# Kernel optimization log

Hardware: AMD Instinct MI355X
Metric: run time of the kernel (lower is better)

The kernel has to match this reference:

```python
import jax, jax.numpy as jnp
import numpy as np

STRIDES = [8, 16, 32, 64, 128]
FEAT_SIZES = [(100, 100), (50, 50), (25, 25), (13, 13), (7, 7)]
IMG_H, IMG_W = 800, 800
NUM_CLASSES = 8  # required by the repeat(8) in _loss_single_scale
BATCH, NUM_GT = 8, 50


def _make_anchor_levels():
    """RetinaNet anchors: octave_base_scale=4, scales_per_octave=3, ratios [0.5,1,2]."""
    ratios = np.array([0.5, 1.0, 2.0], dtype=np.float64)
    scales = 4.0 * 2.0 ** (np.arange(3) / 3.0)
    levels = []
    for stride, (fh, fw) in zip(STRIDES, FEAT_SIZES):
        h_r = np.sqrt(ratios)
        w_r = 1.0 / h_r
        ws = (w_r[:, None] * scales[None, :]).reshape(-1) * stride  # [9]
        hs = (h_r[:, None] * scales[None, :]).reshape(-1) * stride
        base = np.stack([-ws / 2, -hs / 2, ws / 2, hs / 2], axis=1)  # [9,4]
        xs = np.arange(fw) * stride
        ys = np.arange(fh) * stride
        xx, yy = np.meshgrid(xs, ys)  # [fh,fw]
        shifts = np.stack([xx, yy, xx, yy], axis=-1).reshape(-1, 4)  # [fh*fw,4]
        anchors = (shifts[:, None, :] + base[None, :, :]).reshape(-1, 4)  # loc-major, A inner
        levels.append(anchors.astype(np.float32))
    return levels


def _pairwise_iou(a, b):
    # a: [K,4], b: [G,4] -> [K,G]
    area_a = (a[:, 2] - a[:, 0]) * (a[:, 3] - a[:, 1])
    area_b = (b[:, 2] - b[:, 0]) * (b[:, 3] - b[:, 1])
    lt = jnp.maximum(a[:, None, :2], b[None, :, :2])
    rb = jnp.minimum(a[:, None, 2:], b[None, :, 2:])
    wh = jnp.clip(rb - lt, 0.0)
    inter = wh[..., 0] * wh[..., 1]
    return inter / (area_a[:, None] + area_b[None, :] - inter)


def _encode(anchors, gts):
    # DeltaXYWH encode, means=0, stds=1
    aw = anchors[:, 2] - anchors[:, 0]
    ah = anchors[:, 3] - anchors[:, 1]
    ax = anchors[:, 0] + 0.5 * aw
    ay = anchors[:, 1] + 0.5 * ah
    gw = gts[:, 2] - gts[:, 0]
    gh = gts[:, 3] - gts[:, 1]
    gx = gts[:, 0] + 0.5 * gw
    gy = gts[:, 1] + 0.5 * gh
    return jnp.stack([(gx - ax) / aw, (gy - ay) / ah,
                      jnp.log(gw / aw), jnp.log(gh / ah)], axis=1)


def _targets_per_image(anchors, tgt_boxes, tgt_cls):
    # MaxIoUMatcher(thresholds=[0.4,0.5], labels=[0,-1,1], low_quality=True)
    inside = ((anchors[:, 0] >= 0) & (anchors[:, 1] >= 0)
              & (anchors[:, 2] <= IMG_W) & (anchors[:, 3] <= IMG_H))
    iou = _pairwise_iou(anchors, tgt_boxes)             # [K,G]
    iou = jnp.where(inside[:, None], iou, -1.0)          # exclude outside anchors
    max_iou = iou.max(axis=1)
    argmax_gt = iou.argmax(axis=1)
    label = jnp.where(max_iou >= 0.5, 1, jnp.where(max_iou >= 0.4, -1, 0))
    gt_max = iou.max(axis=0)                             # [G]
    is_lq = (iou == gt_max[None, :]) & (gt_max[None, :] > 0)
    any_lq = is_lq.any(axis=1)
    G = tgt_boxes.shape[0]
    lq_gt = jnp.where(is_lq, jnp.arange(G)[None, :], -1).max(axis=1)
    matched_gt = jnp.where(any_lq, lq_gt, argmax_gt)
    label = jnp.where(any_lq, 1, label)
    pos = (label == 1) & inside
    neg = (label == 0) & inside
    deltas = _encode(anchors, tgt_boxes[matched_gt])     # [K,4]
    bbox_targets = jnp.where(pos[:, None], deltas, 0.0)
    bbox_weights = jnp.where(pos[:, None], 1.0, 0.0) * jnp.ones((1, 4), jnp.float32)
    labels_out = jnp.where(pos, tgt_cls[matched_gt].astype(jnp.float32), 0.0)
    label_weights = (pos | neg).astype(jnp.float32)
    return labels_out, label_weights, bbox_targets, bbox_weights, pos.sum(), neg.sum()


def _bce_logits(x, t):
    return jnp.maximum(x, 0.0) - x * t + jnp.log1p(jnp.exp(-jnp.abs(x)))


def _loss_level(cls_out, reg_out, labels, lw, bt, bw, num_samples):
    labels = labels.reshape(-1)
    lw = lw.reshape(-1)
    C = NUM_CLASSES
    cls_score = cls_out.transpose(0, 2, 3, 1).reshape(labels.shape[0], C)  # [N*H*W*A, C]
    tgt = jax.nn.one_hot(labels.astype(jnp.int32), C + 1, dtype=jnp.float32)[:, :C]
    lw2 = jnp.tile(lw, 8).reshape(-1, C)  # faithful to label_weights.repeat(8).reshape(-1, C)
    loss_cls = (_bce_logits(cls_score, tgt) * lw2).sum() / num_samples
    bt = bt.reshape(-1, 4)
    bw = bw.reshape(-1, 4)
    pred = reg_out.transpose(0, 2, 3, 1).reshape(-1, 4)
    loss_bbox = (jnp.abs(pred - bt) * bw).sum() / num_samples
    return loss_cls, loss_bbox


def setup_inputs() -> dict:
    key = jax.random.key(0)
    ks = jax.random.split(key, 16)
    inp = {}
    for i, (fh, fw) in enumerate(FEAT_SIZES):
        inp[f"cls{i}"] = jax.random.normal(ks[i], (BATCH, 9 * NUM_CLASSES, fh, fw), jnp.float32)
        inp[f"reg{i}"] = jax.random.normal(ks[5 + i], (BATCH, 9 * 4, fh, fw), jnp.float32)
    xy = jax.random.uniform(ks[10], (BATCH, NUM_GT, 2), minval=0.0, maxval=600.0)
    wh = jax.random.uniform(ks[11], (BATCH, NUM_GT, 2), minval=20.0, maxval=180.0)
    inp["target_boxes"] = jnp.concatenate([xy, xy + wh], axis=-1).astype(jnp.float32)
    inp["target_class_ids"] = jax.random.randint(ks[12], (BATCH, NUM_GT), 0, NUM_CLASSES, jnp.int64 if jax.config.jax_enable_x64 else jnp.int32)
    return inp


def reference(cls0, cls1, cls2, cls3, cls4, reg0, reg1, reg2, reg3, reg4,
              target_boxes, target_class_ids):
    anchor_levels = _make_anchor_levels()
    anchors = jnp.asarray(np.concatenate(anchor_levels, axis=0))  # [K,4]
    num_lvl = [a.shape[0] for a in anchor_levels]
    labels, lw, bt, bw, npos, nneg = jax.vmap(
        lambda b, c: _targets_per_image(anchors, b, c))(target_boxes, target_class_ids)
    num_samples = (npos.sum() + nneg.sum()).astype(jnp.float32)
    offs = np.cumsum([0] + num_lvl)
    cls_outs = [cls0, cls1, cls2, cls3, cls4]
    reg_outs = [reg0, reg1, reg2, reg3, reg4]
    loss_cls_all = jnp.float32(0.0)
    loss_bbox_all = jnp.float32(0.0)
    for i in range(len(num_lvl)):
        s, e = int(offs[i]), int(offs[i + 1])
        lc, lb = _loss_level(cls_outs[i], reg_outs[i], labels[:, s:e], lw[:, s:e],
                             bt[:, s:e], bw[:, s:e], num_samples)
        loss_cls_all = loss_cls_all + lc
        loss_bbox_all = loss_bbox_all + lb
    return loss_cls_all, loss_bbox_all
```

## Files before the change

kernel.cpp:

```cpp
#include <hip/hip_runtime.h>
#include <cstdint>

#define DEVINL __device__ __forceinline__

constexpr int NB = 8;
constexpr int NG = 50;
constexpr int KTOT = 120087;
constexpr int BK = NB * KTOT;

constexpr int L_W[5]   = {100, 50, 25, 13, 7};
constexpr int L_K[5]   = {90000, 22500, 5625, 1521, 441};
constexpr int L_OFF[5] = {0, 90000, 112500, 118125, 119646};
constexpr int L_WSB[5] = {0, 720000, 900000, 945000, 957168};

constexpr double HR_T[3] = {0.7071067811865476, 1.0, 1.4142135623730951};
constexpr double WR_T[3] = {1.0 / HR_T[0], 1.0, 1.0 / HR_T[2]};
constexpr double SC_T[3] = {4.0, 5.039684199579493, 6.3496042078727974};

__device__ float4 g_anc[KTOT];
__device__ double g_accs[256][2];
__device__ unsigned g_ns;
__device__ unsigned g_done;
__device__ unsigned g_gtmax[NB * NG];
__device__ int8_t g_lab[BK];
__device__ __align__(8) int8_t g_lw[BK];
__device__ int8_t g_pos[BK];
__device__ int8_t g_mg[BK];

DEVINL unsigned encf(float f) {
  unsigned u = __float_as_uint(f);
  return (u & 0x80000000u) ? ~u : (u | 0x80000000u);
}
DEVINL int lvl_of(int k) {
  return (k < 90000) ? 0 : (k < 112500) ? 1 : (k < 118125) ? 2 : (k < 119646) ? 3 : 4;
}
DEVINL float iou_one(float ax0, float ay0, float ax1, float ay1, float areaA,
                     float bx0, float by0, float bx1, float by1, float areaB) {
  float ltx = fmaxf(ax0, bx0);
  float lty = fmaxf(ay0, by0);
  float rbx = fminf(ax1, bx1);
  float rby = fminf(ay1, by1);
  float wx = fmaxf(rbx - ltx, 0.0f);
  float wy = fmaxf(rby - lty, 0.0f);
  float inter = wx * wy;
  return __fdividef(inter, areaA + areaB - inter);
}

DEVINL void wh_f64(int l, int a, double& wsz, double& hsz) {
  int st = 8 << l;
  int ridx = a / 3, sidx = a - ridx * 3;
  double sc = (sidx == 0) ? SC_T[0] : (sidx == 1) ? SC_T[1] : SC_T[2];
  double wr = (ridx == 0) ? WR_T[0] : (ridx == 1) ? WR_T[1] : WR_T[2];
  double hr = (ridx == 0) ? HR_T[0] : (ridx == 1) ? HR_T[1] : HR_T[2];
  wsz = wr * sc * (double)st;
  hsz = hr * sc * (double)st;
}
DEVINL void anchor_from_wh(int l, int xi, int yi, double wsz, double hsz,
                           float& x0, float& y0, float& x1, float& y1) {
  int st = 8 << l;
  double cx = (double)(xi * st), cy = (double)(yi * st);
  x0 = (float)(cx - wsz * 0.5);
  y0 = (float)(cy - hsz * 0.5);
  x1 = (float)(cx + wsz * 0.5);
  y1 = (float)(cy + hsz * 0.5);
}

constexpr int NBLK_ANC = (KTOT + 255) / 256;

DEVINL int axis_cand(int xi, int i0, int lo, int hi, int Wm1) {
  int c;
  if (xi < 4) c = i0 - 1 + xi;
  else if (xi == 4) c = lo;
  else if (xi == 5) c = lo + 1;
  else if (xi == 6) c = hi - 1;
  else if (xi == 7) c = hi;
  else if (xi == 8) c = 0;
  else c = Wm1;
  return min(max(c, 0), Wm1);
}

__global__ __launch_bounds__(256) void k_setup(const float* __restrict__ tb) {
  if (blockIdx.x < NBLK_ANC) {
    if (blockIdx.x == 0) {
      int t = threadIdx.x;
      g_accs[t][0] = 0.0;
      g_accs[t][1] = 0.0;
      if (t == 0) { g_ns = 0u; g_done = 0u; }
    }
    int k = blockIdx.x * 256 + threadIdx.x;
    if (k >= KTOT) return;
    int l = lvl_of(k);
    int r = k - L_OFF[l];
    int loc = r / 9;
    int a = r - loc * 9;
    int W = L_W[l];
    int y = loc / W;
    int x = loc - y * W;
    double wsz, hsz;
    wh_f64(l, a, wsz, hsz);
    float x0, y0, x1, y1;
    anchor_from_wh(l, x, y, wsz, hsz, x0, y0, x1, y1);
    g_anc[k] = make_float4(x0, y0, x1, y1);
    return;
  }
  const int bg = blockIdx.x - NBLK_ANC;
  float4 v = reinterpret_cast<const float4*>(tb)[bg];
  const float bx0 = v.x, by0 = v.y, bx1 = v.z, by1 = v.w;
  const float areaB = (bx1 - bx0) * (by1 - by0);
  const float bcx = 0.5f * (bx0 + bx1), bcy = 0.5f * (by0 + by1);

  float m = -1.0f;
  for (int t = threadIdx.x; t < 4500; t += 256) {
    int l = t / 900;
    int rem = t - l * 900;
    int a = rem / 100;
    int rem2 = rem - a * 100;
    int xi = rem2 / 10;
    int yi = rem2 - xi * 10;
    int W = (l == 0) ? 100 : (l == 1) ? 50 : (l == 2) ? 25 : (l == 3) ? 13 : 7;
    float stf = (float)(8 << l);
    double wsz, hsz;
    wh_f64(l, a, wsz, hsz);
    float whalf = (float)(wsz * 0.5);
    float hhalf = (float)(hsz * 0.5);
    int i0x = (int)floorf(bcx / stf);
    int lox = (int)ceilf(whalf / stf);
    int hix = (int)floorf((800.0f - whalf) / stf);
    int i0y = (int)floorf(bcy / stf);
    int loy = (int)ceilf(hhalf / stf);
    int hiy = (int)floorf((800.0f - hhalf) / stf);
    int cx = axis_cand(xi, i0x, lox, hix, W - 1);
    int cy = axis_cand(yi, i0y, loy, hiy, W - 1);
    float ax0, ay0, ax1, ay1;
    anchor_from_wh(l, cx, cy, wsz, hsz, ax0, ay0, ax1, ay1);
    bool inside = (ax0 >= 0.0f) & (ay0 >= 0.0f) & (ax1 <= 800.0f) & (ay1 <= 800.0f);
    float areaA = (ax1 - ax0) * (ay1 - ay0);
    float iou = inside ? iou_one(ax0, ay0, ax1, ay1, areaA,
                                 bx0, by0, bx1, by1, areaB)
                       : -1.0f;
    m = fmaxf(m, iou);
  }
#pragma unroll
  for (int off = 32; off; off >>= 1) m = fmaxf(m, __shfl_down(m, off));
  __shared__ float s_m[4];
  int lane = threadIdx.x & 63, wid = threadIdx.x >> 6;
  if (lane == 0) s_m[wid] = m;
  __syncthreads();
  if (threadIdx.x == 0) {
    float r = fmaxf(fmaxf(s_m[0], s_m[1]), fmaxf(s_m[2], s_m[3]));
    g_gtmax[bg] = encf(r);
  }
}

constexpr int APB = 4;
__global__ __launch_bounds__(256) void k_assign(const float* __restrict__ tb,
                                                const int* __restrict__ tcls) {
  const int b = blockIdx.y;
  __shared__ float s_b[NG][8];
  __shared__ int s_cls[NG];
  __shared__ unsigned s_cnt;
  int tid = threadIdx.x;
  if (tid == 0) s_cnt = 0u;
  if (tid < NG) {
    float4 v = reinterpret_cast<const float4*>(tb)[b * NG + tid];
    s_b[tid][0] = v.x; s_b[tid][1] = v.y; s_b[tid][2] = v.z; s_b[tid][3] = v.w;
    s_b[tid][4] = (v.z - v.x) * (v.w - v.y);
    unsigned gm = g_gtmax[b * NG + tid];
    s_b[tid][5] = (gm > 0x80000000u) ? __uint_as_float(gm ^ 0x80000000u)
                                     : __uint_as_float(0x7FC00000u);
    s_cls[tid] = tcls[b * NG + tid];
  }
  __syncthreads();

  const int base = (blockIdx.x * 256 + tid) * APB;
  float Ax0[APB], Ay0[APB], Ax1[APB], Ay1[APB], areaA[APB];
  bool inside[APB];
  float ex0 = __builtin_inff(), ey0 = __builtin_inff();
  float ex1 = -__builtin_inff(), ey1 = -__builtin_inff();
#pragma unroll
  for (int ap = 0; ap < APB; ++ap) {
    int k = base + ap;
    bool valid = k < KTOT;
    float4 A = g_anc[valid ? k : 0];
    bool ins = valid & (A.x >= 0.0f) & (A.y >= 0.0f) & (A.z <= 800.0f) & (A.w <= 800.0f);
    inside[ap] = ins;
    ex0 = fminf(ex0, ins ? A.x : __builtin_inff());
    ey0 = fminf(ey0, ins ? A.y : __builtin_inff());
    ex1 = fmaxf(ex1, ins ? A.z : -__builtin_inff());
    ey1 = fmaxf(ey1, ins ? A.w : -__builtin_inff());
    if (!ins) A = make_float4(-4000.0f, -4000.0f, -3999.0f, -3999.0f);
    Ax0[ap] = A.x; Ay0[ap] = A.y; Ax1[ap] = A.z; Ay1[ap] = A.w;
    areaA[ap] = (A.z - A.x) * (A.w - A.y);
  }
#pragma unroll
  for (int off = 1; off < 64; off <<= 1) {
    ex0 = fminf(ex0, __shfl_xor(ex0, off));
    ey0 = fminf(ey0, __shfl_xor(ey0, off));
    ex1 = fmaxf(ex1, __shfl_xor(ex1, off));
    ey1 = fmaxf(ey1, __shfl_xor(ey1, off));
  }
  unsigned long long amask;
  {
    int g = tid & 63;
    bool act = false;
    if (g < NG) {
      float ox = fminf(ex1, s_b[g][2]) - fmaxf(ex0, s_b[g][0]);
      float oy = fminf(ey1, s_b[g][3]) - fmaxf(ey0, s_b[g][1]);
      act = (ox > 0.0f) && (oy > 0.0f);
    }
    amask = __ballot(act);
  }

  float best[APB];
  int arg[APB], lqg[APB];
#pragma unroll
  for (int ap = 0; ap < APB; ++ap) { best[ap] = -2.0f; arg[ap] = 0; lqg[ap] = -1; }

  while (amask) {
    int g = __builtin_ctzll(amask);
    amask &= amask - 1;
    float gx0 = s_b[g][0], gy0 = s_b[g][1], gx1 = s_b[g][2], gy1 = s_b[g][3];
    float gar = s_b[g][4], qmx = s_b[g][5];
#pragma unroll
    for (int ap = 0; ap < APB; ++ap) {
      float iou = iou_one(Ax0[ap], Ay0[ap], Ax1[ap], Ay1[ap], areaA[ap],
                          gx0, gy0, gx1, gy1, gar);
      if (iou > best[ap]) { best[ap] = iou; arg[ap] = g; }
      if (iou == qmx) lqg[ap] = g;
    }
  }

  int cnt = 0;
#pragma unroll
  for (int ap = 0; ap < APB; ++ap) {
    int k = base + ap;
    if (k < KTOT) {
      int lab = (best[ap] >= 0.5f) ? 1 : ((best[ap] >= 0.4f) ? -1 : 0);
      int mg = arg[ap];
      if (lqg[ap] >= 0) { lab = 1; mg = lqg[ap]; }
      bool pos = (lab == 1) && inside[ap];
      bool neg = (lab == 0) && inside[ap];
      int l = lvl_of(k);
      int r = k - L_OFF[l];
      int widx = L_WSB[l] + b * L_K[l] + r;
      g_lab[widx] = pos ? (int8_t)s_cls[mg] : (int8_t)0;
      g_lw[widx] = (pos || neg) ? 1 : 0;
      g_pos[widx] = pos ? 1 : 0;
      g_mg[widx] = (int8_t)mg;
      cnt += (pos || neg) ? 1 : 0;
    }
  }
#pragma unroll
  for (int off = 32; off; off >>= 1) cnt += __shfl_down(cnt, off);
  if ((tid & 63) == 0 && cnt) atomicAdd(&s_cnt, (unsigned)cnt);
  __syncthreads();
  if (tid == 0 && s_cnt) atomicAdd(&g_ns, s_cnt);
}

constexpr int G_OFF[6] = {0, 180000, 225000, 236304, 239400, 240336};
constexpr int TOTAL_G = 240336;

template <int HW, int GPL, int KL, int WSB, int LOFF>
DEVINL void level_term4(const float* __restrict__ cls, const float* __restrict__ reg,
                        const float4* __restrict__ tb4, int j, float& vc, float& vb) {
  constexpr int NPG = 9 * GPL;
  int b = j / NPG;
  int rem = j - b * NPG;
  int a = rem / GPL;
  int gi = rem - a * GPL;
  int pix0 = gi * 4;
  const float* cb = cls + (b * 72 + a * 8) * HW + pix0;
  const int8_t* lwb = g_lw + WSB + 8 * (9 * pix0 + a);
  int idxb = WSB + b * KL + 9 * pix0 + a;

  if (pix0 + 4 <= HW) {
    float xs[8][4];
#pragma unroll
    for (int c = 0; c < 8; ++c) {
      float4 v4 = *reinterpret_cast<const float4*>(cb + c * HW);
      xs[c][0] = v4.x; xs[c][1] = v4.y; xs[c][2] = v4.z; xs[c][3] = v4.w;
    }
#pragma unroll
    for (int e = 0; e < 4; ++e) {
      unsigned long long lwq =
          *reinterpret_cast<const unsigned long long*>(lwb + 72 * e);
      if (lwq) {
        int lab = g_lab[idxb + 9 * e];
#pragma unroll
        for (int c = 0; c < 8; ++c) {
          float w = (float)((unsigned)(lwq >> (8 * c)) & 0xffu);
          float x = xs[c][e];
          float t = (lab == c) ? 1.0f : 0.0f;
          float ax = fabsf(x);
          float ex = __expf(-ax);
          vc += (fmaxf(x, 0.0f) - x * t + __logf(1.0f + ex)) * w;
        }
      }
      if (g_pos[idxb + 9 * e]) {
        int mg = g_mg[idxb + 9 * e];
        int q = (pix0 + e) * 9 + a;
        float4 A = g_anc[LOFF + q];
        float aw = A.z - A.x, ah = A.w - A.y;
        float acx = A.x + 0.5f * aw, acy = A.y + 0.5f * ah;
        float4 gb = tb4[b * NG + mg];
        float gw = gb.z - gb.x, gh = gb.w - gb.y;
        float gcx = gb.x + 0.5f * gw, gcy = gb.y + 0.5f * gh;
        const float* rbase = reg + (b * 36 + a * 4) * HW + pix0 + e;
        vb += fabsf(rbase[0] - (gcx - acx) / aw);
        vb += fabsf(rbase[HW] - (gcy - acy) / ah);
        vb += fabsf(rbase[2 * HW] - logf(gw / aw));
        vb += fabsf(rbase[3 * HW] - logf(gh / ah));
      }
    }
  } else {
    int nrem = HW - pix0;
#pragma unroll
    for (int e = 0; e < 3; ++e) {
      if (e < nrem) {
        unsigned long long lwq =
            *reinterpret_cast<const unsigned long long*>(lwb + 72 * e);
        if (lwq) {
          int lab = g_lab[idxb + 9 * e];
#pragma unroll
          for (int c = 0; c < 8; ++c) {
            float w = (float)((unsigned)(lwq >> (8 * c)) & 0xffu);
            float x = cb[c * HW + e];
            float t = (lab == c) ? 1.0f : 0.0f;
            float ax = fabsf(x);
            float ex = __expf(-ax);
            vc += (fmaxf(x, 0.0f) - x * t + __logf(1.0f + ex)) * w;
          }
        }
        if (g_pos[idxb + 9 * e]) {
          int mg = g_mg[idxb + 9 * e];
          int q = (pix0 + e) * 9 + a;
          float4 A = g_anc[LOFF + q];
          float aw = A.z - A.x, ah = A.w - A.y;
          float acx = A.x + 0.5f * aw, acy = A.y + 0.5f * ah;
          float4 gb = tb4[b * NG + mg];
          float gw = gb.z - gb.x, gh = gb.w - gb.y;
          float gcx = gb.x + 0.5f * gw, gcy = gb.y + 0.5f * gh;
          const float* rbase = reg + (b * 36 + a * 4) * HW + pix0 + e;
          vb += fabsf(rbase[0] - (gcx - acx) / aw);
          vb += fabsf(rbase[HW] - (gcy - acy) / ah);
          vb += fabsf(rbase[2 * HW] - logf(gw / aw));
          vb += fabsf(rbase[3 * HW] - logf(gh / ah));
        }
      }
    }
  }
}

__global__ __launch_bounds__(256) void k_loss(
    const float* __restrict__ c0, const float* __restrict__ c1,
    const float* __restrict__ c2, const float* __restrict__ c3,
    const float* __restrict__ c4, const float* __restrict__ r0,
    const float* __restrict__ r1, const float* __restrict__ r2,
    const float* __restrict__ r3, const float* __restrict__ r4,
    const float* __restrict__ tb, float* __restrict__ out) {
  const float4* tb4 = reinterpret_cast<const float4*>(tb);
  int T = blockIdx.x * 256 + threadIdx.x;
  float vc = 0.0f, vb = 0.0f;
  if (T < TOTAL_G) {
    if (T < G_OFF[1])      level_term4<10000, 2500, 90000, 0, 0>(c0, r0, tb4, T, vc, vb);
    else if (T < G_OFF[2]) level_term4<2500, 625, 22500, 720000, 90000>(c1, r1, tb4, T - G_OFF[1], vc, vb);
    else if (T < G_OFF[3]) level_term4<625, 157, 5625, 900000, 112500>(c2, r2, tb4, T - G_OFF[2], vc, vb);
    else if (T < G_OFF[4]) level_term4<169, 43, 1521, 945000, 118125>(c3, r3, tb4, T - G_OFF[3], vc, vb);
    else                   level_term4<49, 13, 441, 957168, 119646>(c4, r4, tb4, T - G_OFF[4], vc, vb);
  }
#pragma unroll
  for (int off = 32; off; off >>= 1) {
    vc += __shfl_down(vc, off);
    vb += __shfl_down(vb, off);
  }
  __shared__ float sc_[4], sb_[4];
  __shared__ bool s_last;
  int lane = threadIdx.x & 63;
  int wid = threadIdx.x >> 6;
  if (lane == 0) { sc_[wid] = vc; sb_[wid] = vb; }
  __syncthreads();
  if (threadIdx.x == 0) {
    float tc = sc_[0] + sc_[1] + sc_[2] + sc_[3];
    float tbx = sb_[0] + sb_[1] + sb_[2] + sb_[3];
    int slot = blockIdx.x & 255;
    if (tc != 0.0f) atomicAdd(&g_accs[slot][0], (double)tc);
    if (tbx != 0.0f) atomicAdd(&g_accs[slot][1], (double)tbx);
    __threadfence();
    unsigned old = atomicAdd(&g_done, 1u);
    s_last = (old == gridDim.x - 1);
  }
  __syncthreads();
  if (s_last) {
    int t = threadIdx.x;
    double a0 = atomicAdd(&g_accs[t][0], 0.0);
    double a1 = atomicAdd(&g_accs[t][1], 0.0);
#pragma unroll
    for (int off = 32; off; off >>= 1) {
      a0 += __shfl_down(a0, off);
      a1 += __shfl_down(a1, off);
    }
    __shared__ double s0[4], s1[4];
    if (lane == 0) { s0[wid] = a0; s1[wid] = a1; }
    __syncthreads();
    if (t == 0) {
      double A0 = s0[0] + s0[1] + s0[2] + s0[3];
      double A1 = s1[0] + s1[1] + s1[2] + s1[3];
      double n = (double)g_ns;
      out[0] = (float)(A0 / n);
      out[1] = (float)(A1 / n);
    }
  }
}

extern "C" void kernel_launch(void* const* d_in, const int* in_sizes, int n_in,
                              void* d_out, int out_size, void* d_ws, size_t ws_size,
                              hipStream_t stream) {
  const float* c0 = (const float*)d_in[0];
  const float* r0 = (const float*)d_in[1];
  const float* c1 = (const float*)d_in[2];
  const float* r1 = (const float*)d_in[3];
  const float* c2 = (const float*)d_in[4];
  const float* r2 = (const float*)d_in[5];
  const float* c3 = (const float*)d_in[6];
  const float* r3 = (const float*)d_in[7];
  const float* c4 = (const float*)d_in[8];
  const float* r4 = (const float*)d_in[9];
  const float* tb = (const float*)d_in[10];
  const int* tcls = (const int*)d_in[11];
  float* out = (float*)d_out;

  k_setup<<<dim3(NBLK_ANC + NB * NG), dim3(256), 0, stream>>>(tb);
  k_assign<<<dim3((KTOT + 256 * APB - 1) / (256 * APB), NB), dim3(256), 0, stream>>>(tb, tcls);
  k_loss<<<dim3((TOTAL_G + 255) / 256), dim3(256), 0, stream>>>(c0, c1, c2, c3, c4,
                                                                r0, r1, r2, r3, r4, tb, out);
}
```

Before: 173.2 us.

## Split loss kernel into per-channel classification threads and separate box-loss threads

The fused per-anchor-group loss work is replaced by a finer thread decomposition. Each thread now handles one class channel over four pixels using vectorized loads for the two large levels, or a single element for the small levels. A separate range of threads computes the box-regression loss over anchors in groups of four. This raises parallelism and removes the 32-value register array and divergent positive-anchor work from the classification path. In exchange the label and weight bytes are re-read once per channel, and the launch grows to several times as many threads.

```diff
diff --git a/kernel.cpp b/kernel.cpp
--- a/kernel.cpp
+++ b/kernel.cpp
@@ -257,96 +257,89 @@
   if (tid == 0 && s_cnt) atomicAdd(&g_ns, s_cnt);
 }
 
-constexpr int G_OFF[6] = {0, 180000, 225000, 236304, 239400, 240336};
-constexpr int TOTAL_G = 240336;
-
-template <int HW, int GPL, int KL, int WSB, int LOFF>
-DEVINL void level_term4(const float* __restrict__ cls, const float* __restrict__ reg,
-                        const float4* __restrict__ tb4, int j, float& vc, float& vb) {
-  constexpr int NPG = 9 * GPL;
+constexpr int VT0 = 1440000;
+constexpr int VT1 = 360000;
+constexpr int V_TOT = VT0 + VT1;
+constexpr int ST2 = 360000, ST3 = 97344, ST4 = 28224;
+constexpr int S_TOT = ST2 + ST3 + ST4;
+constexpr int BT0 = 180000, BT1 = 45000, BT2 = 11256, BT3 = 3048, BT4 = 888;
+constexpr int B_TOT = BT0 + BT1 + BT2 + BT3 + BT4;
+constexpr int LOSS_THREADS = V_TOT + S_TOT + B_TOT;
+constexpr int LOSS_BLOCKS = (LOSS_THREADS + 255) / 256;
+
+DEVINL float bce_one(float x, int lab, int c) {
+  float t = (lab == c) ? 1.0f : 0.0f;
+  float ax = fabsf(x);
+  float ex = __expf(-ax);
+  return fmaxf(x, 0.0f) - x * t + __logf(1.0f + ex);
+}
+
+template <int HW, int KL, int WSB>
+DEVINL void cls_vec(const float* __restrict__ cls, int j, float& vc) {
+  constexpr int GPL = HW / 4;
+  constexpr int NPG = 72 * GPL;
   int b = j / NPG;
   int rem = j - b * NPG;
-  int a = rem / GPL;
-  int gi = rem - a * GPL;
+  int ch = rem / GPL;
+  int gi = rem - ch * GPL;
+  int a = ch >> 3, c = ch & 7;
   int pix0 = gi * 4;
-  const float* cb = cls + (b * 72 + a * 8) * HW + pix0;
-  const int8_t* lwb = g_lw + WSB + 8 * (9 * pix0 + a);
-  int idxb = WSB + b * KL + 9 * pix0 + a;
-
-  if (pix0 + 4 <= HW) {
-    float xs[8][4];
-#pragma unroll
-    for (int c = 0; c < 8; ++c) {
-      float4 v4 = *reinterpret_cast<const float4*>(cb + c * HW);
-      xs[c][0] = v4.x; xs[c][1] = v4.y; xs[c][2] = v4.z; xs[c][3] = v4.w;
-    }
-#pragma unroll
-    for (int e = 0; e < 4; ++e) {
-      unsigned long long lwq =
-          *reinterpret_cast<const unsigned long long*>(lwb + 72 * e);
-      if (lwq) {
-        int lab = g_lab[idxb + 9 * e];
-#pragma unroll
-        for (int c = 0; c < 8; ++c) {
-          float w = (float)((unsigned)(lwq >> (8 * c)) & 0xffu);
-          float x = xs[c][e];
-          float t = (lab == c) ? 1.0f : 0.0f;
-          float ax = fabsf(x);
-          float ex = __expf(-ax);
-          vc += (fmaxf(x, 0.0f) - x * t + __logf(1.0f + ex)) * w;
-        }
-      }
-      if (g_pos[idxb + 9 * e]) {
-        int mg = g_mg[idxb + 9 * e];
-        int q = (pix0 + e) * 9 + a;
-        float4 A = g_anc[LOFF + q];
-        float aw = A.z - A.x, ah = A.w - A.y;
-        float acx = A.x + 0.5f * aw, acy = A.y + 0.5f * ah;
-        float4 gb = tb4[b * NG + mg];
-        float gw = gb.z - gb.x, gh = gb.w - gb.y;
-        float gcx = gb.x + 0.5f * gw, gcy = gb.y + 0.5f * gh;
-        const float* rbase = reg + (b * 36 + a * 4) * HW + pix0 + e;
-        vb += fabsf(rbase[0] - (gcx - acx) / aw);
-        vb += fabsf(rbase[HW] - (gcy - acy) / ah);
-        vb += fabsf(rbase[2 * HW] - logf(gw / aw));
-        vb += fabsf(rbase[3 * HW] - logf(gh / ah));
-      }
-    }
-  } else {
-    int nrem = HW - pix0;
-#pragma unroll
-    for (int e = 0; e < 3; ++e) {
-      if (e < nrem) {
-        unsigned long long lwq =
-            *reinterpret_cast<const unsigned long long*>(lwb + 72 * e);
-        if (lwq) {
-          int lab = g_lab[idxb + 9 * e];
-#pragma unroll
-          for (int c = 0; c < 8; ++c) {
-            float w = (float)((unsigned)(lwq >> (8 * c)) & 0xffu);
-            float x = cb[c * HW + e];
-            float t = (lab == c) ? 1.0f : 0.0f;
-            float ax = fabsf(x);
-            float ex = __expf(-ax);
-            vc += (fmaxf(x, 0.0f) - x * t + __logf(1.0f + ex)) * w;
-          }
-        }
-        if (g_pos[idxb + 9 * e]) {
-          int mg = g_mg[idxb + 9 * e];
-          int q = (pix0 + e) * 9 + a;
-          float4 A = g_anc[LOFF + q];
-          float aw = A.z - A.x, ah = A.w - A.y;
-          float acx = A.x + 0.5f * aw, acy = A.y + 0.5f * ah;
-          float4 gb = tb4[b * NG + mg];
-          float gw = gb.z - gb.x, gh = gb.w - gb.y;
-          float gcx = gb.x + 0.5f * gw, gcy = gb.y + 0.5f * gh;
-          const float* rbase = reg + (b * 36 + a * 4) * HW + pix0 + e;
-          vb += fabsf(rbase[0] - (gcx - acx) / aw);
-          vb += fabsf(rbase[HW] - (gcy - acy) / ah);
-          vb += fabsf(rbase[2 * HW] - logf(gw / aw));
-          vb += fabsf(rbase[3 * HW] - logf(gh / ah));
-        }
-      }
+  float4 v4 = *reinterpret_cast<const float4*>(cls + (b * 72 + ch) * HW + pix0);
+  float xs[4] = {v4.x, v4.y, v4.z, v4.w};
+  int qb = pix0 * 9 + a;
+  int ib = WSB + b * KL + qb;
+#pragma unroll
+  for (int e = 0; e < 4; ++e) {
+    float w = (float)g_lw[WSB + 8 * (qb + 9 * e) + c];
+    if (w != 0.0f) {
+      int lab = g_lab[ib + 9 * e];
+      vc += bce_one(xs[e], lab, c);
+    }
+  }
+}
+
+template <int HW, int KL, int WSB>
+DEVINL void cls_scalar(const float* __restrict__ cls, int j, float& vc) {
+  constexpr int NPE = 72 * HW;
+  int b = j / NPE;
+  int rem = j - b * NPE;
+  int ch = rem / HW;
+  int pix = rem - ch * HW;
+  int a = ch >> 3, c = ch & 7;
+  int q = pix * 9 + a;
+  float w = (float)g_lw[WSB + 8 * q + c];
+  if (w != 0.0f) {
+    float x = cls[(b * 72 + ch) * HW + pix];
+    int lab = g_lab[WSB + b * KL + q];
+    vc += bce_one(x, lab, c);
+  }
+}
+
+template <int HW, int KL, int WSB, int LOFF, int GRP>
+DEVINL void box_grp(const float* __restrict__ reg, const float4* __restrict__ tb4,
+                    int j, float& vb) {
+  int b = j / GRP;
+  int gi = j - b * GRP;
+  int q0 = gi * 4;
+  int nval = (q0 + 4 <= KL) ? 4 : (KL - q0);
+#pragma unroll
+  for (int e = 0; e < 4; ++e) {
+    if (e < nval && g_pos[WSB + b * KL + q0 + e]) {
+      int q = q0 + e;
+      int mg = g_mg[WSB + b * KL + q];
+      int pix = q / 9;
+      int a = q - pix * 9;
+      float4 A = g_anc[LOFF + q];
+      float aw = A.z - A.x, ah = A.w - A.y;
+      float acx = A.x + 0.5f * aw, acy = A.y + 0.5f * ah;
+      float4 gb = tb4[b * NG + mg];
+      float gw = gb.z - gb.x, gh = gb.w - gb.y;
+      float gcx = gb.x + 0.5f * gw, gcy = gb.y + 0.5f * gh;
+      const float* rbase = reg + (b * 36 + a * 4) * HW + pix;
+      vb += fabsf(rbase[0] - (gcx - acx) / aw);
+      vb += fabsf(rbase[HW] - (gcy - acy) / ah);
+      vb += fabsf(rbase[2 * HW] - logf(gw / aw));
+      vb += fabsf(rbase[3 * HW] - logf(gh / ah));
     }
   }
 }
@@ -361,12 +354,22 @@
   const float4* tb4 = reinterpret_cast<const float4*>(tb);
   int T = blockIdx.x * 256 + threadIdx.x;
   float vc = 0.0f, vb = 0.0f;
-  if (T < TOTAL_G) {
-    if (T < G_OFF[1])      level_term4<10000, 2500, 90000, 0, 0>(c0, r0, tb4, T, vc, vb);
-    else if (T < G_OFF[2]) level_term4<2500, 625, 22500, 720000, 90000>(c1, r1, tb4, T - G_OFF[1], vc, vb);
-    else if (T < G_OFF[3]) level_term4<625, 157, 5625, 900000, 112500>(c2, r2, tb4, T - G_OFF[2], vc, vb);
-    else if (T < G_OFF[4]) level_term4<169, 43, 1521, 945000, 118125>(c3, r3, tb4, T - G_OFF[3], vc, vb);
-    else                   level_term4<49, 13, 441, 957168, 119646>(c4, r4, tb4, T - G_OFF[4], vc, vb);
+  if (T < VT0) {
+    cls_vec<10000, 90000, 0>(c0, T, vc);
+  } else if (T < V_TOT) {
+    cls_vec<2500, 22500, 720000>(c1, T - VT0, vc);
+  } else if (T < V_TOT + S_TOT) {
+    int t2 = T - V_TOT;
+    if (t2 < ST2)            cls_scalar<625, 5625, 900000>(c2, t2, vc);
+    else if (t2 < ST2 + ST3) cls_scalar<169, 1521, 945000>(c3, t2 - ST2, vc);
+    else                     cls_scalar<49, 441, 957168>(c4, t2 - ST2 - ST3, vc);
+  } else if (T < LOSS_THREADS) {
+    int t3 = T - V_TOT - S_TOT;
+    if (t3 < BT0)                        box_grp<10000, 90000, 0, 0, 22500>(r0, tb4, t3, vb);
+    else if (t3 < BT0 + BT1)             box_grp<2500, 22500, 720000, 90000, 5625>(r1, tb4, t3 - BT0, vb);
+    else if (t3 < BT0 + BT1 + BT2)       box_grp<625, 5625, 900000, 112500, 1407>(r2, tb4, t3 - BT0 - BT1, vb);
+    else if (t3 < BT0 + BT1 + BT2 + BT3) box_grp<169, 1521, 945000, 118125, 381>(r3, tb4, t3 - BT0 - BT1 - BT2, vb);
+    else                                 box_grp<49, 441, 957168, 119646, 111>(r4, tb4, t3 - BT0 - BT1 - BT2 - BT3, vb);
   }
 #pragma unroll
   for (int off = 32; off; off >>= 1) {
@@ -431,6 +434,6 @@
 
   k_setup<<<dim3(NBLK_ANC + NB * NG), dim3(256), 0, stream>>>(tb);
   k_assign<<<dim3((KTOT + 256 * APB - 1) / (256 * APB), NB), dim3(256), 0, stream>>>(tb, tcls);
-  k_loss<<<dim3((TOTAL_G + 255) / 256), dim3(256), 0, stream>>>(c0, c1, c2, c3, c4,
-                                                                r0, r1, r2, r3, r4, tb, out);
-}
+  k_loss<<<dim3(LOSS_BLOCKS), dim3(256), 0, stream>>>(c0, c1, c2, c3, c4,
+                                                      r0, r1, r2, r3, r4, tb, out);
+}
```

Result: slower. 423.8 us (+144.7%).

## Store assignment targets in tensor order and use one thread per anchor slot

Applied to the files above, without the earlier changes.

The assignment kernel now writes label, positive flag and matched-gt arrays indexed in the prediction tensor's (batch, anchor, pixel) order, and scatters the label-weight bytes into a matching permuted layout. The loss kernel drops the 4-pixel-per-thread float4 scheme and launches one thread per anchor slot, so consecutive threads read consecutive pixels of the class and regression tensors. This aims to make target and prediction reads coalesced and to remove the tail-handling branch. In exchange it launches about four times as many threads, gives up float4 vector loads, and makes the assign-side writes scattered. The odd lw indexing, which mixes batch into the 8-byte grouping, looks fragile.

```diff
diff --git a/kernel.cpp b/kernel.cpp
--- a/kernel.cpp
+++ b/kernel.cpp
@@ -242,11 +242,23 @@
       bool neg = (lab == 0) && inside[ap];
       int l = lvl_of(k);
       int r = k - L_OFF[l];
-      int widx = L_WSB[l] + b * L_K[l] + r;
-      g_lab[widx] = pos ? (int8_t)s_cls[mg] : (int8_t)0;
-      g_lw[widx] = (pos || neg) ? 1 : 0;
-      g_pos[widx] = pos ? 1 : 0;
-      g_mg[widx] = (int8_t)mg;
+      int KL = (l == 0) ? 90000 : (l == 1) ? 22500 : (l == 2) ? 5625
+               : (l == 3) ? 1521 : 441;
+      int HWl = (l == 0) ? 10000 : (l == 1) ? 2500 : (l == 2) ? 625
+                : (l == 3) ? 169 : 49;
+      int WSB = (l == 0) ? 0 : (l == 1) ? 720000 : (l == 2) ? 900000
+                : (l == 3) ? 945000 : 957168;
+      int pix = r / 9;
+      int a = r - pix * 9;
+      int tIdx = WSB + b * KL + a * HWl + pix;
+      g_lab[tIdx] = pos ? (int8_t)s_cls[mg] : (int8_t)0;
+      g_pos[tIdx] = pos ? 1 : 0;
+      g_mg[tIdx] = (int8_t)mg;
+      int p = b * KL + r;
+      int q = p >> 3, c = p & 7;
+      int pixq = q / 9;
+      int aq = q - pixq * 9;
+      g_lw[WSB + 8 * (aq * HWl + pixq) + c] = (pos || neg) ? 1 : 0;
       cnt += (pos || neg) ? 1 : 0;
     }
   }
@@ -257,97 +269,47 @@
   if (tid == 0 && s_cnt) atomicAdd(&g_ns, s_cnt);
 }
 
-constexpr int G_OFF[6] = {0, 180000, 225000, 236304, 239400, 240336};
-constexpr int TOTAL_G = 240336;
-
-template <int HW, int GPL, int KL, int WSB, int LOFF>
-DEVINL void level_term4(const float* __restrict__ cls, const float* __restrict__ reg,
-                        const float4* __restrict__ tb4, int j, float& vc, float& vb) {
-  constexpr int NPG = 9 * GPL;
-  int b = j / NPG;
-  int rem = j - b * NPG;
-  int a = rem / GPL;
-  int gi = rem - a * GPL;
-  int pix0 = gi * 4;
-  const float* cb = cls + (b * 72 + a * 8) * HW + pix0;
-  const int8_t* lwb = g_lw + WSB + 8 * (9 * pix0 + a);
-  int idxb = WSB + b * KL + 9 * pix0 + a;
-
-  if (pix0 + 4 <= HW) {
-    float xs[8][4];
+constexpr int S_CUM1 = 720000, S_CUM2 = 900000, S_CUM3 = 945000, S_CUM4 = 957168;
+constexpr int LOSS_BLOCKS = (BK + 255) / 256;
+
+template <int HW, int KL, int WSB, int LOFF>
+DEVINL void slot_term(const float* __restrict__ cls, const float* __restrict__ reg,
+                      const float4* __restrict__ tb4, int j, float& vc, float& vb) {
+  int b = j / KL;
+  int s = j - b * KL;
+  int a = s / HW;
+  int pix = s - a * HW;
+  int tIdx = WSB + b * KL + a * HW + pix;
+
+  unsigned long long lwq =
+      *reinterpret_cast<const unsigned long long*>(&g_lw[WSB + 8 * (a * HW + pix)]);
+  if (lwq) {
+    int lab = g_lab[tIdx];
+    const float* cb = cls + (b * 72 + a * 8) * HW + pix;
 #pragma unroll
     for (int c = 0; c < 8; ++c) {
-      float4 v4 = *reinterpret_cast<const float4*>(cb + c * HW);
-      xs[c][0] = v4.x; xs[c][1] = v4.y; xs[c][2] = v4.z; xs[c][3] = v4.w;
-    }
-#pragma unroll
-    for (int e = 0; e < 4; ++e) {
-      unsigned long long lwq =
-          *reinterpret_cast<const unsigned long long*>(lwb + 72 * e);
-      if (lwq) {
-        int lab = g_lab[idxb + 9 * e];
-#pragma unroll
-        for (int c = 0; c < 8; ++c) {
-          float w = (float)((unsigned)(lwq >> (8 * c)) & 0xffu);
-          float x = xs[c][e];
-          float t = (lab == c) ? 1.0f : 0.0f;
-          float ax = fabsf(x);
-          float ex = __expf(-ax);
-          vc += (fmaxf(x, 0.0f) - x * t + __logf(1.0f + ex)) * w;
-        }
-      }
-      if (g_pos[idxb + 9 * e]) {
-        int mg = g_mg[idxb + 9 * e];
-        int q = (pix0 + e) * 9 + a;
-        float4 A = g_anc[LOFF + q];
-        float aw = A.z - A.x, ah = A.w - A.y;
-        float acx = A.x + 0.5f * aw, acy = A.y + 0.5f * ah;
-        float4 gb = tb4[b * NG + mg];
-        float gw = gb.z - gb.x, gh = gb.w - gb.y;
-        float gcx = gb.x + 0.5f * gw, gcy = gb.y + 0.5f * gh;
-        const float* rbase = reg + (b * 36 + a * 4) * HW + pix0 + e;
-        vb += fabsf(rbase[0] - (gcx - acx) / aw);
-        vb += fabsf(rbase[HW] - (gcy - acy) / ah);
-        vb += fabsf(rbase[2 * HW] - logf(gw / aw));
-        vb += fabsf(rbase[3 * HW] - logf(gh / ah));
-      }
-    }
-  } else {
-    int nrem = HW - pix0;
-#pragma unroll
-    for (int e = 0; e < 3; ++e) {
-      if (e < nrem) {
-        unsigned long long lwq =
-            *reinterpret_cast<const unsigned long long*>(lwb + 72 * e);
-        if (lwq) {
-          int lab = g_lab[idxb + 9 * e];
-#pragma unroll
-          for (int c = 0; c < 8; ++c) {
-            float w = (float)((unsigned)(lwq >> (8 * c)) & 0xffu);
-            float x = cb[c * HW + e];
-            float t = (lab == c) ? 1.0f : 0.0f;
-            float ax = fabsf(x);
-            float ex = __expf(-ax);
-            vc += (fmaxf(x, 0.0f) - x * t + __logf(1.0f + ex)) * w;
-          }
-        }
-        if (g_pos[idxb + 9 * e]) {
-          int mg = g_mg[idxb + 9 * e];
-          int q = (pix0 + e) * 9 + a;
-          float4 A = g_anc[LOFF + q];
-          float aw = A.z - A.x, ah = A.w - A.y;
-          float acx = A.x + 0.5f * aw, acy = A.y + 0.5f * ah;
-          float4 gb = tb4[b * NG + mg];
-          float gw = gb.z - gb.x, gh = gb.w - gb.y;
-          float gcx = gb.x + 0.5f * gw, gcy = gb.y + 0.5f * gh;
-          const float* rbase = reg + (b * 36 + a * 4) * HW + pix0 + e;
-          vb += fabsf(rbase[0] - (gcx - acx) / aw);
-          vb += fabsf(rbase[HW] - (gcy - acy) / ah);
-          vb += fabsf(rbase[2 * HW] - logf(gw / aw));
-          vb += fabsf(rbase[3 * HW] - logf(gh / ah));
-        }
-      }
-    }
+      float w = (float)((unsigned)(lwq >> (8 * c)) & 0xffu);
+      float x = cb[c * HW];
+      float t = (lab == c) ? 1.0f : 0.0f;
+      float ax = fabsf(x);
+      float ex = __expf(-ax);
+      vc += (fmaxf(x, 0.0f) - x * t + __logf(1.0f + ex)) * w;
+    }
+  }
+  if (g_pos[tIdx]) {
+    int mg = g_mg[tIdx];
+    int q = pix * 9 + a;
+    float4 A = g_anc[LOFF + q];
+    float aw = A.z - A.x, ah = A.w - A.y;
+    float acx = A.x + 0.5f * aw, acy = A.y + 0.5f * ah;
+    float4 gb = tb4[b * NG + mg];
+    float gw = gb.z - gb.x, gh = gb.w - gb.y;
+    float gcx = gb.x + 0.5f * gw, gcy = gb.y + 0.5f * gh;
+    const float* rbase = reg + (b * 36 + a * 4) * HW + pix;
+    vb += fabsf(rbase[0] - (gcx - acx) / aw);
+    vb += fabsf(rbase[HW] - (gcy - acy) / ah);
+    vb += fabsf(rbase[2 * HW] - logf(gw / aw));
+    vb += fabsf(rbase[3 * HW] - logf(gh / ah));
   }
 }
 
@@ -361,13 +323,12 @@
   const float4* tb4 = reinterpret_cast<const float4*>(tb);
   int T = blockIdx.x * 256 + threadIdx.x;
   float vc = 0.0f, vb = 0.0f;
-  if (T < TOTAL_G) {
-    if (T < G_OFF[1])      level_term4<10000, 2500, 90000, 0, 0>(c0, r0, tb4, T, vc, vb);
-    else if (T < G_OFF[2]) level_term4<2500, 625, 22500, 720000, 90000>(c1, r1, tb4, T - G_OFF[1], vc, vb);
-    else if (T < G_OFF[3]) level_term4<625, 157, 5625, 900000, 112500>(c2, r2, tb4, T - G_OFF[2], vc, vb);
-    else if (T < G_OFF[4]) level_term4<169, 43, 1521, 945000, 118125>(c3, r3, tb4, T - G_OFF[3], vc, vb);
-    else                   level_term4<49, 13, 441, 957168, 119646>(c4, r4, tb4, T - G_OFF[4], vc, vb);
-  }
+  if (T < S_CUM1)      slot_term<10000, 90000, 0, 0>(c0, r0, tb4, T, vc, vb);
+  else if (T < S_CUM2) slot_term<2500, 22500, 720000, 90000>(c1, r1, tb4, T - S_CUM1, vc, vb);
+  else if (T < S_CUM3) slot_term<625, 5625, 900000, 112500>(c2, r2, tb4, T - S_CUM2, vc, vb);
+  else if (T < S_CUM4) slot_term<169, 1521, 945000, 118125>(c3, r3, tb4, T - S_CUM3, vc, vb);
+  else if (T < BK)     slot_term<49, 441, 957168, 119646>(c4, r4, tb4, T - S_CUM4, vc, vb);
+
 #pragma unroll
   for (int off = 32; off; off >>= 1) {
     vc += __shfl_down(vc, off);
@@ -431,6 +392,6 @@
 
   k_setup<<<dim3(NBLK_ANC + NB * NG), dim3(256), 0, stream>>>(tb);
   k_assign<<<dim3((KTOT + 256 * APB - 1) / (256 * APB), NB), dim3(256), 0, stream>>>(tb, tcls);
-  k_loss<<<dim3((TOTAL_G + 255) / 256), dim3(256), 0, stream>>>(c0, c1, c2, c3, c4,
-                                                                r0, r1, r2, r3, r4, tb, out);
-}
+  k_loss<<<dim3(LOSS_BLOCKS), dim3(256), 0, stream>>>(c0, c1, c2, c3, c4,
+                                                      r0, r1, r2, r3, r4, tb, out);
+}
```

After: 220.1 us. 27.1% more time.
